# Kernel optimization log

Measured on AMD Instinct MI355X. Metric: run time of the kernel, lower is better.

## Reference

```python
import jax, jax.numpy as jnp
import numpy as np
jax.config.update("jax_enable_x64", True)  # RoPE is applied in float64 in the original

NH, NKV, HD, ROT = 32, 8, 64, 32


def _rope(x, cos, sin):
    # x: [B,h,S,HD]; cos/sin: [B,1,S,ROT//2] (float64)
    x = x.astype(jnp.float64)
    x_rot, x_pass = x[..., :ROT], x[..., ROT:]
    r, i = x_rot[..., :ROT // 2], x_rot[..., ROT // 2:]
    o_r = r * cos - i * sin
    o_i = r * sin + i * cos
    out = jnp.stack((o_r, o_i), axis=-1).reshape(x.shape[:-1] + (ROT,))
    return jnp.concatenate([out, x_pass], axis=-1)


def setup_inputs() -> dict:
    key = jax.random.key(0)
    ks = jax.random.split(key, 16)
    B, S, H, I = 1, 2048, 2048, 8192
    f = jnp.float32
    s = 0.02
    qkv_dim = NH * HD + 2 * NKV * HD  # 3072
    d = {}
    d["hidden_states"] = jax.random.normal(ks[0], (B, S, H), f)
    d["position_ids"] = jnp.arange(B * S, dtype=jnp.int64).reshape(B, S)
    d["cos"] = jax.random.uniform(ks[1], (B, 1, S, ROT // 2), f)
    d["sin"] = jax.random.uniform(ks[2], (B, 1, S, ROT // 2), f)
    d["ln_w"] = jnp.ones((H,), f)
    d["ln_b"] = jnp.zeros((H,), f)
    d["wq"] = jax.random.normal(ks[3], (H, NH * HD), f) * s
    d["wk"] = jax.random.normal(ks[4], (H, NKV * HD), f) * s
    d["wv"] = jax.random.normal(ks[5], (H, NKV * HD), f) * s
    d["wo"] = jax.random.normal(ks[6], (NH * HD, H), f) * s
    d["tau_wq"] = jax.random.normal(ks[7], (qkv_dim, NH), f) * s
    d["tau_wv"] = jax.random.normal(ks[8], (qkv_dim, NH), f) * s
    d["tau_alpha"] = jax.random.normal(ks[9], (NH,), f) * s
    d["up_w"] = jax.random.normal(ks[10], (H, I), f) * s
    d["up_b"] = jnp.zeros((I,), f)
    d["down_w"] = jax.random.normal(ks[11], (I, H), f) * s
    d["down_b"] = jnp.zeros((H,), f)
    return d


def reference(hidden_states, position_ids, cos, sin, ln_w, ln_b, wq, wk, wv, wo,
              tau_wq, tau_wv, tau_alpha, up_w, up_b, down_w, down_b):
    B, S, H = hidden_states.shape
    eps = 1e-5
    # input_layernorm (shared by parallel attn + mlp branches)
    mu = hidden_states.mean(-1, keepdims=True)
    var = hidden_states.var(-1, keepdims=True)
    xn = (hidden_states - mu) / jnp.sqrt(var + eps) * ln_w + ln_b

    # ---- attention with tau gating ----
    q = xn @ wq          # [B,S,NH*HD]
    k = xn @ wk          # [B,S,NKV*HD]
    v = xn @ wv
    qkv = jnp.concatenate([q, k, v], axis=-1)
    tok = jax.nn.gelu(qkv, approximate=False)  # F.gelu default (erf)
    tok_q = jnp.tanh(tok @ tau_wq).transpose(0, 2, 1)  # [B,NH,S]
    tok_v = jnp.tanh(tok @ tau_wv).transpose(0, 2, 1)
    pos = position_ids.astype(tok_q.dtype) + 1
    tau_pos = 1 + (jax.nn.sigmoid(tau_alpha[None, :, None] * jnp.log(pos)[:, None, :]) - 0.5)
    tau_q = (tok_q + tau_pos)[..., None]  # [B,NH,S,1]
    tau_v = (tok_v + tau_pos)[..., None]

    qh = q.reshape(B, S, NH, HD).transpose(0, 2, 1, 3) * tau_q
    kh = k.reshape(B, S, NKV, HD).transpose(0, 2, 1, 3)
    vh = v.reshape(B, S, NKV, HD).transpose(0, 2, 1, 3) * tau_v[:, :NKV]  # repeat-then-slice == first NKV heads

    cos64 = cos.astype(jnp.float64)
    sin64 = sin.astype(jnp.float64)
    qh = _rope(qh, cos64, sin64).astype(jnp.float32)
    kh = _rope(kh, cos64, sin64).astype(jnp.float32)

    g = NH // NKV
    kh = jnp.repeat(kh, g, axis=1)  # GQA expand [B,NKV,S,D] -> [B,NH,S,D]
    vh = jnp.repeat(vh, g, axis=1)

    scores = jnp.einsum('bhqd,bhkd->bhqk', qh, kh) / jnp.sqrt(jnp.float32(HD))
    causal = jnp.tril(jnp.ones((S, S), dtype=bool))
    scores = jnp.where(causal, scores, jnp.float32(-1e9))
    p = jax.nn.softmax(scores, axis=-1)
    attn = jnp.einsum('bhqk,bhkd->bhqd', p, vh)
    attn = attn.transpose(0, 2, 1, 3).reshape(B, S, NH * HD)
    attn_out = attn @ wo

    # ---- dense MLP (gelu_pytorch_tanh, ungated) ----
    h = jax.nn.gelu(xn @ up_w + up_b, approximate=True)
    mlp_out = h @ down_w + down_b

    return hidden_states + attn_out + mlp_out
```

## Files before the change

kernel.cpp:

```cpp
#include <hip/hip_runtime.h>
#include <hip/hip_bf16.h>
#include <math.h>

typedef __bf16 bf16;
typedef bf16 bf16x4 __attribute__((ext_vector_type(4)));
typedef bf16 bf16x8 __attribute__((ext_vector_type(8)));
typedef float f32x4 __attribute__((ext_vector_type(4)));

#define AS1 __attribute__((address_space(1)))
#define AS3 __attribute__((address_space(3)))

__global__ __launch_bounds__(256) void k_transpose(const float* __restrict__ src,
                                                   bf16* __restrict__ dst,
                                                   int R, int C, int dstStride) {
    __shared__ float tile[32][33];
    int bc = blockIdx.x * 32, br = blockIdx.y * 32;
    int tx = threadIdx.x & 31, ty = threadIdx.x >> 5;
    for (int i = 0; i < 4; i++) {
        int r = ty + i * 8;
        tile[r][tx] = src[(size_t)(br + r) * C + bc + tx];
    }
    __syncthreads();
    for (int i = 0; i < 4; i++) {
        int r = ty + i * 8;
        dst[(size_t)(bc + r) * dstStride + br + tx] = (bf16)tile[tx][r];
    }
}

__global__ __launch_bounds__(256) void k_ln(const float* __restrict__ x,
                                            const float* __restrict__ w,
                                            const float* __restrict__ b,
                                            bf16* __restrict__ xn) {
    int s = blockIdx.x;
    int t = threadIdx.x;
    const float* row = x + (size_t)s * 2048;
    const float4* r4 = (const float4*)row;
    float4 A = r4[t * 2], B = r4[t * 2 + 1];
    float sum = A.x + A.y + A.z + A.w + B.x + B.y + B.z + B.w;
    float sq = A.x * A.x + A.y * A.y + A.z * A.z + A.w * A.w +
               B.x * B.x + B.y * B.y + B.z * B.z + B.w * B.w;
    for (int off = 32; off; off >>= 1) {
        sum += __shfl_down(sum, off);
        sq  += __shfl_down(sq, off);
    }
    __shared__ float rs[4], rq[4];
    if ((t & 63) == 0) { rs[t >> 6] = sum; rq[t >> 6] = sq; }
    __syncthreads();
    float S = rs[0] + rs[1] + rs[2] + rs[3];
    float Q = rq[0] + rq[1] + rq[2] + rq[3];
    float mu = S * (1.0f / 2048.0f);
    float var = Q * (1.0f / 2048.0f) - mu * mu;
    float rstd = rsqrtf(var + 1e-5f);
    float vals[8] = {A.x, A.y, A.z, A.w, B.x, B.y, B.z, B.w};
    bf16x8 ov;
    int j0 = t * 8;
    for (int i = 0; i < 8; i++)
        ov[i] = (bf16)((vals[i] - mu) * rstd * w[j0 + i] + b[j0 + i]);
    *(bf16x8*)&xn[(size_t)s * 2048 + j0] = ov;
}

template <int MODE>
__global__ __launch_bounds__(256) void k_gemm(const bf16* __restrict__ A,
                                              const bf16* __restrict__ Bt,
                                              int M, int N, int K, int kslice,
                                              float* __restrict__ Cf,
                                              bf16* __restrict__ Cb,
                                              const float* __restrict__ bias) {
    __shared__ bf16 As[2][128][64];
    __shared__ bf16 Bs[2][128][64];
    int t = threadIdx.x;
    int bm = blockIdx.y, bn = blockIdx.x, bz = blockIdx.z;
    int w = t >> 6, l = t & 63, lr = l & 15, lg = l >> 4;
    int wm = w >> 1, wn = w & 1;
    f32x4 acc[4][4] = {};
    const bf16* Ab = A + (size_t)(bm * 128) * K + (size_t)bz * kslice;
    const bf16* Bb = Bt + (size_t)(bn * 128) * K + (size_t)bz * kslice;
    int srow = t >> 3;
    int scol = ((t & 7) ^ (srow & 7)) * 8;
    int nkt = kslice >> 6;

    auto STAGE = [&](int kt, int buf) {
        int k0 = kt * 64;
#pragma unroll
        for (int i = 0; i < 4; i++) {
            const bf16* ga = Ab + (size_t)(i * 32 + srow) * K + k0 + scol;
            const bf16* gb = Bb + (size_t)(i * 32 + srow) * K + k0 + scol;
            char* la = (char*)(&As[buf][0][0]) + i * 4096 + w * 1024;
            char* lb = (char*)(&Bs[buf][0][0]) + i * 4096 + w * 1024;
            __builtin_amdgcn_global_load_lds(
                (const AS1 void*)ga, (AS3 void*)la, 16, 0, 0);
            __builtin_amdgcn_global_load_lds(
                (const AS1 void*)gb, (AS3 void*)lb, 16, 0, 0);
        }
    };

    int sw = (lr & 7) << 4;

    STAGE(0, 0);
    for (int kt = 0; kt < nkt; ++kt) {
        int cur = kt & 1;
        if (kt + 1 < nkt) {
            STAGE(kt + 1, cur ^ 1);
            asm volatile("s_waitcnt vmcnt(8) lgkmcnt(0)" ::: "memory");
        } else {
            asm volatile("s_waitcnt vmcnt(0) lgkmcnt(0)" ::: "memory");
        }
        __builtin_amdgcn_s_barrier();
        asm volatile("" ::: "memory");
        const char* Abase = (const char*)&As[cur][0][0];
        const char* Bbase = (const char*)&Bs[cur][0][0];
#pragma unroll
        for (int kk = 0; kk < 2; kk++) {
            bf16x8 a[4], b[4];
            for (int fm = 0; fm < 4; fm++)
                a[fm] = *(const bf16x8*)(Abase + (wm * 64 + fm * 16 + lr) * 128 +
                                         ((kk * 64 + lg * 16) ^ sw));
            for (int fn = 0; fn < 4; fn++)
                b[fn] = *(const bf16x8*)(Bbase + (wn * 64 + fn * 16 + lr) * 128 +
                                         ((kk * 64 + lg * 16) ^ sw));
            for (int fm = 0; fm < 4; fm++)
                for (int fn = 0; fn < 4; fn++)
                    acc[fm][fn] = __builtin_amdgcn_mfma_f32_16x16x32_bf16(
                        a[fm], b[fn], acc[fm][fn], 0, 0, 0);
        }
        asm volatile("" ::: "memory");
        __builtin_amdgcn_s_barrier();
    }
    float* Cz = Cf + (size_t)bz * M * N;
    for (int fm = 0; fm < 4; fm++)
        for (int fn = 0; fn < 4; fn++) {
            int col = bn * 128 + wn * 64 + fn * 16 + lr;
            for (int r = 0; r < 4; r++) {
                int row = bm * 128 + wm * 64 + fm * 16 + lg * 4 + r;
                size_t idx = (size_t)row * N + col;
                float v = acc[fm][fn][r];
                if constexpr (MODE == 0) {
                    Cz[idx] = v;
                } else {
                    v += bias[col];
                    float g = 0.5f * v * (1.0f + tanhf(0.7978845608028654f *
                                                       (v + 0.044715f * v * v * v)));
                    Cb[idx] = (bf16)g;
                }
            }
        }
}

__global__ __launch_bounds__(256) void k_final(const float* __restrict__ hidden,
                                               const float* __restrict__ w0,
                                               const float* __restrict__ w1,
                                               const float* __restrict__ p0,
                                               const float* __restrict__ p1,
                                               const float* __restrict__ bias,
                                               float* __restrict__ out) {
    int idx = blockIdx.x * 256 + threadIdx.x;
    int col4 = idx & 511;
    float4 b = ((const float4*)bias)[col4];
    float4 h = ((const float4*)hidden)[idx];
    float4 a0 = ((const float4*)w0)[idx];
    float4 a1 = ((const float4*)w1)[idx];
    float4 d0 = ((const float4*)p0)[idx];
    float4 d1 = ((const float4*)p1)[idx];
    float4 o;
    o.x = h.x + a0.x + a1.x + d0.x + d1.x + b.x;
    o.y = h.y + a0.y + a1.y + d0.y + d1.y + b.y;
    o.z = h.z + a0.z + a1.z + d0.z + d1.z + b.z;
    o.w = h.w + a0.w + a1.w + d0.w + d1.w + b.w;
    ((float4*)out)[idx] = o;
}

__global__ __launch_bounds__(256) void k_tau(const float* __restrict__ qkv,
                                             const float* __restrict__ twq,
                                             const float* __restrict__ twv,
                                             const float* __restrict__ alpha,
                                             const int* __restrict__ pos,
                                             float* __restrict__ tauq,
                                             float* __restrict__ tauv) {
    int s = blockIdx.x;
    __shared__ float tok[3072];
    __shared__ float part[4][64];
    const float* row = qkv + (size_t)s * 3072;
    for (int j = threadIdx.x; j < 3072; j += 256) {
        float x = row[j];
        tok[j] = x * 0.5f * (1.0f + erff(x * 0.7071067811865475f));
    }
    __syncthreads();
    int h = threadIdx.x & 63;
    int chunk = threadIdx.x >> 6;
    const float* W = (h < 32) ? twq : twv;
    int hh = h & 31;
    float acc = 0.0f;
    int j0 = chunk * 768;
    for (int j = j0; j < j0 + 768; ++j) acc += tok[j] * W[j * 32 + hh];
    part[chunk][h] = acc;
    __syncthreads();
    if (chunk == 0) {
        float tot = part[0][h] + part[1][h] + part[2][h] + part[3][h];
        float pf = (float)(pos[s] + 1);
        float lp = logf(pf);
        float tp = 1.0f + (1.0f / (1.0f + expf(-alpha[hh] * lp)) - 0.5f);
        float val = tanhf(tot) + tp;
        if (h < 32) tauq[s * 32 + hh] = val;
        else        tauv[s * 32 + hh] = val;
    }
}

__global__ __launch_bounds__(256) void k_heads(const float* __restrict__ qkv,
                                               const float* __restrict__ cosb,
                                               const float* __restrict__ sinb,
                                               const float* __restrict__ tauq,
                                               const float* __restrict__ tauv,
                                               bf16* __restrict__ Qr,
                                               bf16* __restrict__ Kr,
                                               bf16* __restrict__ Vt) {
    int s = blockIdx.x * 4 + (threadIdx.x >> 6);
    int d = threadIdx.x & 63;
    int j = (d >> 1) & 15;
    float c = cosb[s * 16 + j], sn = sinb[s * 16 + j];
    const float* row = qkv + (size_t)s * 3072;
    for (int h = 0; h < 32; ++h) {
        float x = row[h * 64 + d] * tauq[s * 32 + h] * 0.125f;
        float xr = __shfl(x, j);
        float xi = __shfl(x, j + 16);
        float out = (d < 32) ? ((d & 1) ? (xr * sn + xi * c) : (xr * c - xi * sn)) : x;
        Qr[(size_t)s * 2048 + h * 64 + d] = (bf16)out;
    }
    for (int h = 0; h < 8; ++h) {
        float x = row[2048 + h * 64 + d];
        float xr = __shfl(x, j);
        float xi = __shfl(x, j + 16);
        float out = (d < 32) ? ((d & 1) ? (xr * sn + xi * c) : (xr * c - xi * sn)) : x;
        Kr[(size_t)s * 512 + h * 64 + d] = (bf16)out;
    }
    for (int h = 0; h < 8; ++h) {
        float x = row[2560 + h * 64 + d] * tauv[s * 32 + h];
        Vt[((size_t)h * 64 + d) * 2048 + s] = (bf16)x;
    }
}

__global__ __launch_bounds__(512, 4) void k_attn(const bf16* __restrict__ Q,
                                                 const bf16* __restrict__ K,
                                                 const bf16* __restrict__ Vt,
                                                 bf16* __restrict__ O) {
    __shared__ bf16 Ks[2][64][64];
    __shared__ bf16 Vs[2][64][64];
    __shared__ bf16 plds[8][16][72];
    int t = threadIdx.x;
    int w = t >> 6, l = t & 63, lr = l & 15, lg = l >> 4;
    int h = blockIdx.x, kvh = h >> 2;
    int qb = 15 - blockIdx.y;
    int qrow0 = qb * 128 + w * 16;
    int qg = qrow0 + lr;
    int qmax = qrow0 + 15;
    int nkt = 2 * qb + 2;

    int srow = t >> 3;
    int scol = ((t & 7) * 16) ^ ((srow & 7) << 4);
    const char* gK = (const char*)(K + (size_t)kvh * 64);
    const char* gV = (const char*)(Vt + (size_t)kvh * 64 * 2048);
    char* ldsK = (char*)&Ks[0][0][0] + w * 1024;
    char* ldsV = (char*)&Vs[0][0][0] + w * 1024;

    bf16x8 q0 = *(const bf16x8*)&Q[(size_t)qg * 2048 + h * 64 + lg * 8];
    bf16x8 q1 = *(const bf16x8*)&Q[(size_t)qg * 2048 + h * 64 + 32 + lg * 8];
    f32x4 o[4] = {};
    float m = -3e38f, ll = 0.0f;
    int sw = (lr & 7) << 4;

    __builtin_amdgcn_global_load_lds(
        (const AS1 void*)(gK + (size_t)srow * 1024 + scol), (AS3 void*)ldsK, 16, 0, 0);
    __builtin_amdgcn_global_load_lds(
        (const AS1 void*)(gV + (size_t)srow * 4096 + scol), (AS3 void*)ldsV, 16, 0, 0);
    __syncthreads();

    for (int kt = 0; kt < nkt; ++kt) {
        int kb = kt * 64;
        int cur = kt & 1, nxt = cur ^ 1;
        if (kt + 1 < nkt) {
            int kb2 = kb + 64;
            __builtin_amdgcn_global_load_lds(
                (const AS1 void*)(gK + (size_t)(kb2 + srow) * 1024 + scol),
                (AS3 void*)(ldsK + nxt * 8192), 16, 0, 0);
            __builtin_amdgcn_global_load_lds(
                (const AS1 void*)(gV + (size_t)srow * 4096 + kb2 * 2 + scol),
                (AS3 void*)(ldsV + nxt * 8192), 16, 0, 0);
        }
        if (kb <= qmax) {
            const char* Kbuf = (const char*)Ks + cur * 8192;
            const char* Vbuf = (const char*)Vs + cur * 8192;
            f32x4 sc[2][2];
#pragma unroll
            for (int ks = 0; ks < 2; ks++)
                for (int kc = 0; kc < 2; kc++) {
                    int krow = ks * 32 + kc * 16 + lr;
                    bf16x8 k0 = *(const bf16x8*)(Kbuf + krow * 128 + ((lg * 16) ^ sw));
                    bf16x8 k1 = *(const bf16x8*)(Kbuf + krow * 128 + ((64 + lg * 16) ^ sw));
                    f32x4 z = {};
                    z = __builtin_amdgcn_mfma_f32_16x16x32_bf16(k0, q0, z, 0, 0, 0);
                    sc[ks][kc] = __builtin_amdgcn_mfma_f32_16x16x32_bf16(k1, q1, z, 0, 0, 0);
                }
            if (kb + 63 > qrow0) {
#pragma unroll
                for (int ks = 0; ks < 2; ks++)
                    for (int kc = 0; kc < 2; kc++)
                        for (int r = 0; r < 4; r++) {
                            int kg = kb + ks * 32 + kc * 16 + lg * 4 + r;
                            if (kg > qg) sc[ks][kc][r] = -1e30f;
                        }
            }
            float tmax = -3e38f;
#pragma unroll
            for (int ks = 0; ks < 2; ks++)
                for (int kc = 0; kc < 2; kc++)
                    for (int r = 0; r < 4; r++) tmax = fmaxf(tmax, sc[ks][kc][r]);
            tmax = fmaxf(tmax, __shfl_xor(tmax, 16));
            tmax = fmaxf(tmax, __shfl_xor(tmax, 32));
            if (!__all(tmax <= m)) {
                float mn = fmaxf(m, tmax);
                float al = __expf(m - mn);
                m = mn;
                ll *= al;
#pragma unroll
                for (int fn = 0; fn < 4; fn++)
                    for (int r = 0; r < 4; r++) o[fn][r] *= al;
            }
            float rsum = 0.0f;
#pragma unroll
            for (int ks = 0; ks < 2; ks++)
                for (int kc = 0; kc < 2; kc++) {
                    bf16x4 pk;
                    for (int r = 0; r < 4; r++) {
                        float pv = __expf(sc[ks][kc][r] - m);
                        rsum += pv;
                        pk[r] = (bf16)pv;
                    }
                    *(bf16x4*)&plds[w][lr][ks * 32 + kc * 16 + lg * 4] = pk;
                }
            ll += rsum;
            bf16x8 vf[2][4];
#pragma unroll
            for (int ks = 0; ks < 2; ks++)
                for (int fn = 0; fn < 4; fn++) {
                    int drow = fn * 16 + lr;
                    vf[ks][fn] = *(const bf16x8*)(Vbuf + drow * 128 + ((ks * 64 + lg * 16) ^ sw));
                }
            asm volatile("s_waitcnt lgkmcnt(0)" ::: "memory");
            __builtin_amdgcn_sched_barrier(0);
            bf16x8 pa0 = *(const bf16x8*)&plds[w][lr][lg * 8];
            bf16x8 pa1 = *(const bf16x8*)&plds[w][lr][32 + lg * 8];
#pragma unroll
            for (int fn = 0; fn < 4; fn++)
                o[fn] = __builtin_amdgcn_mfma_f32_16x16x32_bf16(vf[0][fn], pa0, o[fn], 0, 0, 0);
#pragma unroll
            for (int fn = 0; fn < 4; fn++)
                o[fn] = __builtin_amdgcn_mfma_f32_16x16x32_bf16(vf[1][fn], pa1, o[fn], 0, 0, 0);
        }
        __syncthreads();
    }

    ll += __shfl_xor(ll, 16);
    ll += __shfl_xor(ll, 32);
    float rinv = 1.0f / ll;
    for (int fn = 0; fn < 4; fn++) {
        bf16x4 ov;
        for (int r = 0; r < 4; r++) ov[r] = (bf16)(o[fn][r] * rinv);
        *(bf16x4*)&O[(size_t)qg * 2048 + h * 64 + fn * 16 + lg * 4] = ov;
    }
}

extern "C" void kernel_launch(void* const* d_in, const int* in_sizes, int n_in,
                              void* d_out, int out_size, void* d_ws, size_t ws_size,
                              hipStream_t stream) {
    const float* hidden = (const float*)d_in[0];
    const int*   pos    = (const int*)d_in[1];
    const float* cosb   = (const float*)d_in[2];
    const float* sinb   = (const float*)d_in[3];
    const float* ln_w   = (const float*)d_in[4];
    const float* ln_b   = (const float*)d_in[5];
    const float* wq     = (const float*)d_in[6];
    const float* wk     = (const float*)d_in[7];
    const float* wv     = (const float*)d_in[8];
    const float* wo     = (const float*)d_in[9];
    const float* twq    = (const float*)d_in[10];
    const float* twv    = (const float*)d_in[11];
    const float* alpha  = (const float*)d_in[12];
    const float* up_w   = (const float*)d_in[13];
    const float* up_b   = (const float*)d_in[14];
    const float* down_w = (const float*)d_in[15];
    const float* down_b = (const float*)d_in[16];
    float* out = (float*)d_out;

    char* p = (char*)d_ws;
    auto alloc = [&](size_t n) -> char* {
        char* r = p;
        p += (n + 255) & ~(size_t)255;
        return r;
    };
    bf16* wqkvT = (bf16*)alloc((size_t)3072 * 2048 * 2);
    bf16* woT   = (bf16*)alloc((size_t)2048 * 2048 * 2);
    bf16* upT   = (bf16*)alloc((size_t)8192 * 2048 * 2);
    bf16* downT = (bf16*)alloc((size_t)2048 * 8192 * 2);
    bf16* xn    = (bf16*)alloc((size_t)2048 * 2048 * 2);
    float* qkv  = (float*)alloc((size_t)2048 * 3072 * 4);
    float* tauq = (float*)alloc((size_t)2048 * 32 * 4);
    float* tauv = (float*)alloc((size_t)2048 * 32 * 4);
    bf16* Qr    = (bf16*)alloc((size_t)2048 * 2048 * 2);
    bf16* Kr    = (bf16*)alloc((size_t)2048 * 512 * 2);
    bf16* Vt    = (bf16*)alloc((size_t)8 * 64 * 2048 * 2);
    bf16* aout  = (bf16*)alloc((size_t)2048 * 2048 * 2);
    bf16* hbuf  = (bf16*)alloc((size_t)2048 * 8192 * 2);
    float* Wp   = (float*)alloc((size_t)2 * 2048 * 2048 * 4);
    float* Pp   = (float*)alloc((size_t)2 * 2048 * 2048 * 4);

    k_transpose<<<dim3(64, 64), 256, 0, stream>>>(wq, wqkvT, 2048, 2048, 2048);
    k_transpose<<<dim3(16, 64), 256, 0, stream>>>(wk, wqkvT + (size_t)2048 * 2048, 2048, 512, 2048);
    k_transpose<<<dim3(16, 64), 256, 0, stream>>>(wv, wqkvT + (size_t)2560 * 2048, 2048, 512, 2048);
    k_transpose<<<dim3(64, 64), 256, 0, stream>>>(wo, woT, 2048, 2048, 2048);
    k_transpose<<<dim3(256, 64), 256, 0, stream>>>(up_w, upT, 2048, 8192, 2048);
    k_transpose<<<dim3(64, 256), 256, 0, stream>>>(down_w, downT, 8192, 2048, 8192);

    k_ln<<<2048, 256, 0, stream>>>(hidden, ln_w, ln_b, xn);

    k_gemm<0><<<dim3(24, 16, 1), 256, 0, stream>>>(xn, wqkvT, 2048, 3072, 2048, 2048,
                                                   qkv, nullptr, nullptr);

    k_tau<<<2048, 256, 0, stream>>>(qkv, twq, twv, alpha, pos, tauq, tauv);
    k_heads<<<512, 256, 0, stream>>>(qkv, cosb, sinb, tauq, tauv, Qr, Kr, Vt);

    k_attn<<<dim3(32, 16), 512, 0, stream>>>(Qr, Kr, Vt, aout);

    k_gemm<0><<<dim3(16, 16, 2), 256, 0, stream>>>(aout, woT, 2048, 2048, 2048, 1024,
                                                   Wp, nullptr, nullptr);
    k_gemm<1><<<dim3(64, 16, 1), 256, 0, stream>>>(xn, upT, 2048, 8192, 2048, 2048,
                                                   nullptr, hbuf, up_b);
    k_gemm<0><<<dim3(16, 16, 2), 256, 0, stream>>>(hbuf, downT, 2048, 2048, 8192, 4096,
                                                   Pp, nullptr, nullptr);
    k_final<<<4096, 256, 0, stream>>>(hidden, Wp, Wp + (size_t)2048 * 2048,
                                      Pp, Pp + (size_t)2048 * 2048, down_b, out);
}
```

Measured before the change: 473.8 us.

## Add 256x256-tile GEMM kernel for MLP up/down projections with 4-way split-K

Adds a 512-thread GEMM kernel with 256x256 tiles, swizzled LDS, double-buffered direct global-to-LDS loads and phased MFMA issue with priority hints. It is used for the MLP up projection (with fused GELU) and the down projection, where split-K goes from 2 to 4 and the extra partials reuse the qkv buffer. The GELU tanh is replaced by an exp-based formula. The larger tiles aim for more operand reuse and fewer global loads, at the cost of fewer blocks, higher register and LDS pressure, and an extra two partial reads in the final sum.

```diff
diff --git a/kernel.cpp b/kernel.cpp
--- a/kernel.cpp
+++ b/kernel.cpp
@@ -138,9 +138,123 @@
                     Cz[idx] = v;
                 } else {
                     v += bias[col];
-                    float g = 0.5f * v * (1.0f + tanhf(0.7978845608028654f *
-                                                       (v + 0.044715f * v * v * v)));
-                    Cb[idx] = (bf16)g;
+                    float e = __expf(1.5957691216057308f * (v + 0.044715f * v * v * v));
+                    float th = 1.0f - 2.0f / (e + 1.0f);
+                    Cb[idx] = (bf16)(0.5f * v * (1.0f + th));
+                }
+            }
+        }
+}
+
+template <int MODE>
+__global__ __launch_bounds__(512, 2) void k_gemm256(const bf16* __restrict__ A,
+                                                    const bf16* __restrict__ Bt,
+                                                    int M, int N, int K, int kslice,
+                                                    float* __restrict__ Cf,
+                                                    float* __restrict__ Cf2,
+                                                    bf16* __restrict__ Cb,
+                                                    const float* __restrict__ bias) {
+    __shared__ bf16 As[2][256][64];
+    __shared__ bf16 Bs[2][256][64];
+    int t = threadIdx.x;
+    int w = t >> 6, l = t & 63, lr = l & 15, lg = l >> 4;
+    int wm = w >> 2, wn = w & 3;
+    int bm = blockIdx.y, bn = blockIdx.x, bz = blockIdx.z;
+    f32x4 acc[8][4] = {};
+    const bf16* Ab = A + (size_t)(bm * 256) * K + (size_t)bz * kslice;
+    const bf16* Bb = Bt + (size_t)(bn * 256) * K + (size_t)bz * kslice;
+    int srow = t >> 3;
+    int scol = ((t & 7) ^ (srow & 7)) * 8;
+    int nkt = kslice >> 6;
+    int sw = (lr & 7) << 4;
+
+    auto STAGE = [&](int kt, int buf) {
+        int k0 = kt * 64;
+#pragma unroll
+        for (int i = 0; i < 4; i++) {
+            const bf16* ga = Ab + (size_t)(i * 64 + srow) * K + k0 + scol;
+            const bf16* gb = Bb + (size_t)(i * 64 + srow) * K + k0 + scol;
+            char* la = (char*)(&As[buf][0][0]) + (i * 64 + w * 8) * 128;
+            char* lb = (char*)(&Bs[buf][0][0]) + (i * 64 + w * 8) * 128;
+            __builtin_amdgcn_global_load_lds(
+                (const AS1 void*)ga, (AS3 void*)la, 16, 0, 0);
+            __builtin_amdgcn_global_load_lds(
+                (const AS1 void*)gb, (AS3 void*)lb, 16, 0, 0);
+        }
+    };
+
+    STAGE(0, 0);
+    asm volatile("s_waitcnt vmcnt(0)" ::: "memory");
+    __builtin_amdgcn_s_barrier();
+    asm volatile("" ::: "memory");
+
+    for (int kt = 0; kt < nkt; ++kt) {
+        int cur = kt & 1;
+        const char* Abase = (const char*)&As[cur][0][0] + (wm * 128) * 128;
+        const char* Bbase = (const char*)&Bs[cur][0][0] + (wn * 64) * 128;
+        bf16x8 a[4][2], b[2][2];
+#pragma unroll
+        for (int ph = 0; ph < 4; ++ph) {
+            const int qm = ph >> 1;
+            const int qn = (ph == 1 || ph == 2) ? 1 : 0;
+            if (ph == 0 || ph == 2) {
+#pragma unroll
+                for (int fm = 0; fm < 4; fm++)
+#pragma unroll
+                    for (int kk = 0; kk < 2; kk++)
+                        a[fm][kk] = *(const bf16x8*)(Abase +
+                            (qm * 64 + fm * 16 + lr) * 128 +
+                            ((kk * 64 + lg * 16) ^ sw));
+            }
+            if (ph != 2) {
+#pragma unroll
+                for (int fn = 0; fn < 2; fn++)
+#pragma unroll
+                    for (int kk = 0; kk < 2; kk++)
+                        b[fn][kk] = *(const bf16x8*)(Bbase +
+                            (qn * 32 + fn * 16 + lr) * 128 +
+                            ((kk * 64 + lg * 16) ^ sw));
+            }
+            if (ph == 0 && kt + 1 < nkt) STAGE(kt + 1, cur ^ 1);
+            __builtin_amdgcn_s_barrier();
+            asm volatile("s_waitcnt lgkmcnt(0)" ::: "memory");
+            __builtin_amdgcn_sched_barrier(0);
+            __builtin_amdgcn_s_setprio(1);
+#pragma unroll
+            for (int fm = 0; fm < 4; fm++)
+#pragma unroll
+                for (int fn = 0; fn < 2; fn++)
+#pragma unroll
+                    for (int kk = 0; kk < 2; kk++)
+                        acc[qm * 4 + fm][qn * 2 + fn] =
+                            __builtin_amdgcn_mfma_f32_16x16x32_bf16(
+                                a[fm][kk], b[fn][kk],
+                                acc[qm * 4 + fm][qn * 2 + fn], 0, 0, 0);
+            __builtin_amdgcn_s_setprio(0);
+            if (ph == 3) asm volatile("s_waitcnt vmcnt(0)" ::: "memory");
+            asm volatile("" ::: "memory");
+            __builtin_amdgcn_s_barrier();
+        }
+    }
+
+    float* Cz = ((bz < 2) ? Cf : Cf2) + (size_t)(bz & 1) * M * N;
+#pragma unroll
+    for (int mi = 0; mi < 8; mi++)
+#pragma unroll
+        for (int ni = 0; ni < 4; ni++) {
+            int col = bn * 256 + wn * 64 + (ni >> 1) * 32 + (ni & 1) * 16 + lr;
+            for (int r = 0; r < 4; r++) {
+                int row = bm * 256 + wm * 128 + (mi >> 2) * 64 + (mi & 3) * 16 +
+                          lg * 4 + r;
+                size_t idx = (size_t)row * N + col;
+                float v = acc[mi][ni][r];
+                if constexpr (MODE == 0) {
+                    Cz[idx] = v;
+                } else {
+                    v += bias[col];
+                    float e = __expf(1.5957691216057308f * (v + 0.044715f * v * v * v));
+                    float th = 1.0f - 2.0f / (e + 1.0f);
+                    Cb[idx] = (bf16)(0.5f * v * (1.0f + th));
                 }
             }
         }
@@ -151,6 +265,8 @@
                                                const float* __restrict__ w1,
                                                const float* __restrict__ p0,
                                                const float* __restrict__ p1,
+                                               const float* __restrict__ p2,
+                                               const float* __restrict__ p3,
                                                const float* __restrict__ bias,
                                                float* __restrict__ out) {
     int idx = blockIdx.x * 256 + threadIdx.x;
@@ -161,11 +277,13 @@
     float4 a1 = ((const float4*)w1)[idx];
     float4 d0 = ((const float4*)p0)[idx];
     float4 d1 = ((const float4*)p1)[idx];
+    float4 d2 = ((const float4*)p2)[idx];
+    float4 d3 = ((const float4*)p3)[idx];
     float4 o;
-    o.x = h.x + a0.x + a1.x + d0.x + d1.x + b.x;
-    o.y = h.y + a0.y + a1.y + d0.y + d1.y + b.y;
-    o.z = h.z + a0.z + a1.z + d0.z + d1.z + b.z;
-    o.w = h.w + a0.w + a1.w + d0.w + d1.w + b.w;
+    o.x = h.x + a0.x + a1.x + d0.x + d1.x + d2.x + d3.x + b.x;
+    o.y = h.y + a0.y + a1.y + d0.y + d1.y + d2.y + d3.y + b.y;
+    o.z = h.z + a0.z + a1.z + d0.z + d1.z + d2.z + d3.z + b.z;
+    o.w = h.w + a0.w + a1.w + d0.w + d1.w + d2.w + d3.w + b.w;
     ((float4*)out)[idx] = o;
 }
 
@@ -411,6 +529,7 @@
     bf16* hbuf  = (bf16*)alloc((size_t)2048 * 8192 * 2);
     float* Wp   = (float*)alloc((size_t)2 * 2048 * 2048 * 4);
     float* Pp   = (float*)alloc((size_t)2 * 2048 * 2048 * 4);
+    float* PpX  = qkv;
 
     k_transpose<<<dim3(64, 64), 256, 0, stream>>>(wq, wqkvT, 2048, 2048, 2048);
     k_transpose<<<dim3(16, 64), 256, 0, stream>>>(wk, wqkvT + (size_t)2048 * 2048, 2048, 512, 2048);
@@ -431,10 +550,11 @@
 
     k_gemm<0><<<dim3(16, 16, 2), 256, 0, stream>>>(aout, woT, 2048, 2048, 2048, 1024,
                                                    Wp, nullptr, nullptr);
-    k_gemm<1><<<dim3(64, 16, 1), 256, 0, stream>>>(xn, upT, 2048, 8192, 2048, 2048,
-                                                   nullptr, hbuf, up_b);
-    k_gemm<0><<<dim3(16, 16, 2), 256, 0, stream>>>(hbuf, downT, 2048, 2048, 8192, 4096,
-                                                   Pp, nullptr, nullptr);
+    k_gemm256<1><<<dim3(32, 8, 1), 512, 0, stream>>>(xn, upT, 2048, 8192, 2048, 2048,
+                                                     nullptr, nullptr, hbuf, up_b);
+    k_gemm256<0><<<dim3(8, 8, 4), 512, 0, stream>>>(hbuf, downT, 2048, 2048, 8192, 2048,
+                                                    Pp, PpX, nullptr, nullptr);
     k_final<<<4096, 256, 0, stream>>>(hidden, Wp, Wp + (size_t)2048 * 2048,
-                                      Pp, Pp + (size_t)2048 * 2048, down_b, out);
-}
+                                      Pp, Pp + (size_t)2048 * 2048,
+                                      PpX, PpX + (size_t)2048 * 2048, down_b, out);
+}
```

After: 482.2 us. Within noise of the previous version (+1.8%).
